# Kernel optimization log

Hardware: AMD Instinct MI355X
Metric: run time of the kernel (lower is better)

## Reference

```python
import jax, jax.numpy as jnp
import numpy as np

NUM_LAYERS = 4  # -> 9 blocks: 4 encoder + bottleneck + 4 decoder
EPS = 1e-6
SQRT2 = float(np.sqrt(2.0))
INV_SQRT3 = float(1.0 / np.sqrt(3.0))


def _block(s, v, W0, W1, Wa, Wb):
    """_SelfInteractionUNet with full_square=False, irreps = Mx0e + Mx1o.

    tensor_square of per-channel (0e+1o):
      0e: s*s ; 0e: |v|^2/sqrt(3) ; 1o: sqrt(2)*s*v ; (2e is produced by e3nn
      but irreps_out has no 2e so the Linear discards it -> omitted here).
    """
    M = s.shape[-1]
    ts0a = s * s                                    # [N, M] 0e
    ts0b = jnp.sum(v * v, axis=-1) * INV_SQRT3      # [N, M] 0e
    ts1 = SQRT2 * s[..., None] * v                  # [N, M, 3] 1o
    s_in = jnp.concatenate([s, ts0a, ts0b], axis=-1)   # [N, 3M]
    v_in = jnp.concatenate([v, ts1], axis=1)           # [N, 2M, 3]
    # irreps-segmented Linear with path (fan-in) normalization
    s2 = (s_in @ W0) * (1.0 / np.sqrt(s_in.shape[-1]))               # [N, Mo]
    v2 = jnp.einsum('ncd,co->nod', v_in, W1) * (1.0 / np.sqrt(v_in.shape[1]))  # [N, Mo, 3]
    Mo = W0.shape[-1]
    # gated MLP on invariants (0e part), silu after each layer
    h = jax.nn.silu((s2 @ Wa) * (1.0 / np.sqrt(Mo)))                 # [N, Mo]
    g = jax.nn.silu((h @ Wb) * (1.0 / np.sqrt(Mo)))                  # [N, 2Mo]
    s2 = s2 * g[:, :Mo]
    v2 = v2 * g[:, Mo:, None]
    return s2, v2


def _eq_layernorm(s, v):
    # scalars: center + RMS normalize; vectors: norm-RMS normalize (equivariant)
    s = s - jnp.mean(s, axis=-1, keepdims=True)
    s = s * jax.lax.rsqrt(jnp.mean(s * s, axis=-1, keepdims=True) + EPS)
    v = v * jax.lax.rsqrt(jnp.mean(v * v, axis=(1, 2), keepdims=True) + EPS)
    return s, v


def _unet(scalars, vectors, W0, W1, Wa, Wb):
    s, v = scalars, vectors
    skips = []
    for i in range(NUM_LAYERS):
        s, v = _block(s, v, W0[i], W1[i], Wa[i], Wb[i])
        s, v = _eq_layernorm(s, v)
        skips.append((s, v))
    s, v = _block(s, v, W0[NUM_LAYERS], W1[NUM_LAYERS], Wa[NUM_LAYERS], Wb[NUM_LAYERS])
    for j in range(NUM_LAYERS):
        ss, vs = skips[NUM_LAYERS - 1 - j]
        s, v = s + ss, v + vs
        k = NUM_LAYERS + 1 + j
        s, v = _block(s, v, W0[k], W1[k], Wa[k], Wb[k])
        if j < NUM_LAYERS - 1:  # no norm on last decoder layer (norm_last=False)
            s, v = _eq_layernorm(s, v)
    N = s.shape[0]
    return jnp.concatenate([s, v.reshape(N, -1)], axis=-1)  # [N, 4M] irreps_array layout


def setup_inputs() -> dict:
    key = jax.random.key(0)
    ks = jax.random.split(key, 6)
    N, M = 16384, 256
    return {
        'scalars': jax.random.normal(ks[0], (N, M), jnp.float32),
        'vectors': jax.random.normal(ks[1], (N, M, 3), jnp.float32),
        'W0': jax.random.normal(ks[2], (9, 3 * M, M), jnp.float32),
        'W1': jax.random.normal(ks[3], (9, 2 * M, M), jnp.float32),
        'Wa': jax.random.normal(ks[4], (9, M, M), jnp.float32),
        'Wb': jax.random.normal(ks[5], (9, M, 2 * M), jnp.float32),
    }


def reference(scalars, vectors, W0, W1, Wa, Wb):
    return _unet(scalars, vectors, W0, W1, Wa, Wb)
```

## Files before the change

kernel.cpp:

```cpp
#include <hip/hip_runtime.h>
#include <hip/hip_bf16.h>
#include <math.h>


typedef __attribute__((ext_vector_type(8))) short bf16x8;
typedef __attribute__((ext_vector_type(4))) short bf16x4;
typedef __attribute__((ext_vector_type(4))) float f32x4;
typedef __attribute__((ext_vector_type(4))) _Float16 f16x4;

__device__ __forceinline__ float bf2f(unsigned short u){
  union { unsigned int i; float f; } x; x.i = ((unsigned int)u) << 16; return x.f;
}
__device__ __forceinline__ unsigned short f2bf(float f){
  union { float f; unsigned int i; } x; x.f = f;
  unsigned int i = x.i;
  return (unsigned short)((i + 0x7fffu + ((i >> 16) & 1u)) >> 16);
}

__device__ __forceinline__ f32x4 ld4f(const float* p){ return *(const f32x4*)p; }
__device__ __forceinline__ f32x4 ld4f(const _Float16* p){
  f16x4 v = *(const f16x4*)p;
  f32x4 r;
  #pragma unroll
  for (int j = 0; j < 4; ++j) r[j] = (float)v[j];
  return r;
}

__global__ __launch_bounds__(256)
void transpose_w(const float* __restrict__ W, unsigned short* __restrict__ Wh,
                 unsigned short* __restrict__ Wl, int K, int Mo){
  __shared__ float tile[32][33];
  const int bi = blockIdx.z;
  const float* Wb = W + (size_t)bi * K * Mo;
  const size_t wo = (size_t)bi * K * Mo;
  const int k0 = blockIdx.x * 32, o0 = blockIdx.y * 32;
  const int tx = threadIdx.x & 31, ty = threadIdx.x >> 5;
  #pragma unroll
  for (int i = 0; i < 4; ++i){
    int k = ty + i * 8;
    tile[k][tx] = Wb[(size_t)(k0 + k) * Mo + o0 + tx];
  }
  __syncthreads();
  #pragma unroll
  for (int i = 0; i < 4; ++i){
    int o = ty + i * 8;
    float f = tile[tx][o];
    unsigned short h = f2bf(f);
    unsigned short l = f2bf(f - bf2f(h));
    Wh[wo + (size_t)(o0 + o) * K + k0 + tx] = h;
    Wl[wo + (size_t)(o0 + o) * K + k0 + tx] = l;
  }
}

__global__ __launch_bounds__(256)
void convert_inputs(const float* __restrict__ s, const float* __restrict__ v,
                    float* __restrict__ st, int NM){
  int i = blockIdx.x * 256 + threadIdx.x;
  if (i >= NM) return;
  st[i] = s[i];
  const float* vp = v + (size_t)i * 3;
  st[(size_t)NM + i]     = vp[0];
  st[(size_t)2 * NM + i] = vp[1];
  st[(size_t)3 * NM + i] = vp[2];
}

template<typename ST, int AMODE, int EPI>
__global__ __launch_bounds__(256)
void gemm_k(const ST* __restrict__ Ap,
            const float* __restrict__ St,
            const unsigned short* __restrict__ Bh,
            const unsigned short* __restrict__ Bl,
            int K, int Mo, int NM, float scale,
            ST* __restrict__ outf,
            const ST* __restrict__ s2g,
            const ST* __restrict__ v2g,
            float* __restrict__ stout,
            float* __restrict__ fout)
{
  __shared__ unsigned short Ah[128][40];
  __shared__ unsigned short Al[128][40];
  __shared__ unsigned short Bhs[128][40];
  __shared__ unsigned short Bls[128][40];
  const int tid  = threadIdx.x;
  const int lane = tid & 63;
  const int wave = tid >> 6;
  const int wrow = (wave >> 1) * 64;
  const int wcol = (wave & 1) * 64;
  const int row0 = blockIdx.x * 128;
  const int col0 = blockIdx.y * 128;
  int dplane = 0;
  if (AMODE == 2){ dplane = blockIdx.z; outf += (size_t)dplane * NM; }

  f32x4 acc[4][4];
  #pragma unroll
  for (int m = 0; m < 4; ++m)
    #pragma unroll
    for (int n = 0; n < 4; ++n) acc[m][n] = (f32x4){0.f, 0.f, 0.f, 0.f};

  for (int k0 = 0; k0 < K; k0 += 32){
    const int seg = k0 >> 8;
    #pragma unroll
    for (int it = 0; it < 4; ++it){
      int idx = tid + it * 256;
      int r   = idx >> 3;
      int c4  = (idx & 7) * 4;
      int gr  = row0 + r;
      int gk  = k0 + c4;
      f32x4 f;
      if (AMODE == 0){
        f = ld4f(Ap + (size_t)gr * K + gk);
      } else {
        int c = gk & 255;
        const size_t o = (size_t)gr * 256 + c;
        if (AMODE == 1){
          if (seg == 0){
            f = *(const f32x4*)(St + o);
          } else if (seg == 1){
            f32x4 x = *(const f32x4*)(St + o);
            #pragma unroll
            for (int j = 0; j < 4; ++j) f[j] = x[j] * x[j];
          } else {
            f32x4 a0 = *(const f32x4*)(St + (size_t)NM + o);
            f32x4 a1 = *(const f32x4*)(St + (size_t)2 * NM + o);
            f32x4 a2 = *(const f32x4*)(St + (size_t)3 * NM + o);
            #pragma unroll
            for (int j = 0; j < 4; ++j)
              f[j] = (a0[j]*a0[j] + a1[j]*a1[j] + a2[j]*a2[j]) * 0.57735026918962576f;
          }
        } else {
          const float* vd = St + (size_t)(1 + dplane) * NM;
          if (seg == 0){
            f = *(const f32x4*)(vd + o);
          } else {
            f32x4 sv = *(const f32x4*)(St + o);
            f32x4 vv = *(const f32x4*)(vd + o);
            #pragma unroll
            for (int j = 0; j < 4; ++j)
              f[j] = 1.41421356237309505f * sv[j] * vv[j];
          }
        }
      }
      bf16x4 hi, lo;
      #pragma unroll
      for (int j = 0; j < 4; ++j){
        unsigned short h = f2bf(f[j]);
        hi[j] = (short)h;
        lo[j] = (short)f2bf(f[j] - bf2f(h));
      }
      *(bf16x4*)(&Ah[r][c4]) = hi;
      *(bf16x4*)(&Al[r][c4]) = lo;
    }
    #pragma unroll
    for (int it = 0; it < 2; ++it){
      int idx = tid + it * 256;
      int r   = idx >> 2;
      int kc  = (idx & 3) * 8;
      const size_t o = (size_t)(col0 + r) * K + k0 + kc;
      *(bf16x8*)(&Bhs[r][kc]) = *(const bf16x8*)(Bh + o);
      *(bf16x8*)(&Bls[r][kc]) = *(const bf16x8*)(Bl + o);
    }
    __syncthreads();

    const int arow = lane & 15;
    const int kq   = (lane >> 4) * 8;
    bf16x8 ah[4], al[4], bh[4], bl[4];
    #pragma unroll
    for (int m = 0; m < 4; ++m){
      ah[m] = *(const bf16x8*)(&Ah[wrow + m*16 + arow][kq]);
      al[m] = *(const bf16x8*)(&Al[wrow + m*16 + arow][kq]);
    }
    #pragma unroll
    for (int n = 0; n < 4; ++n){
      bh[n] = *(const bf16x8*)(&Bhs[wcol + n*16 + arow][kq]);
      bl[n] = *(const bf16x8*)(&Bls[wcol + n*16 + arow][kq]);
    }
    #pragma unroll
    for (int m = 0; m < 4; ++m)
      #pragma unroll
      for (int n = 0; n < 4; ++n){
        acc[m][n] = __builtin_amdgcn_mfma_f32_16x16x32_bf16(ah[m], bh[n], acc[m][n], 0, 0, 0);
        acc[m][n] = __builtin_amdgcn_mfma_f32_16x16x32_bf16(al[m], bh[n], acc[m][n], 0, 0, 0);
        acc[m][n] = __builtin_amdgcn_mfma_f32_16x16x32_bf16(ah[m], bl[n], acc[m][n], 0, 0, 0);
      }
    __syncthreads();
  }

  #pragma unroll
  for (int m = 0; m < 4; ++m){
    #pragma unroll
    for (int n = 0; n < 4; ++n){
      const int cg = col0 + wcol + n * 16 + (lane & 15);
      #pragma unroll
      for (int j = 0; j < 4; ++j){
        const int rg = row0 + wrow + m * 16 + ((lane >> 4) * 4) + j;
        float val = acc[m][n][j] * scale;
        if (EPI == 0){
          outf[(size_t)rg * Mo + cg] = (ST)val;
        } else if (EPI == 1){
          outf[(size_t)rg * Mo + cg] = (ST)(val / (1.f + expf(-val)));
        } else {
          float gv = val / (1.f + expf(-val));
          if (cg < 256){
            float sval = (float)s2g[(size_t)rg * 256 + cg] * gv;
            if (EPI == 2) stout[(size_t)rg * 256 + cg] = sval;
            else          fout[(size_t)rg * 1024 + cg] = sval;
          } else {
            int c = cg - 256;
            #pragma unroll
            for (int d = 0; d < 3; ++d){
              float vv = (float)v2g[(size_t)d * NM + (size_t)rg * 256 + c] * gv;
              if (EPI == 2) stout[(size_t)(1 + d) * NM + (size_t)rg * 256 + c] = vv;
              else          fout[(size_t)rg * 1024 + 256 + 3 * (size_t)c + d] = vv;
            }
          }
        }
      }
    }
  }
}

__global__ __launch_bounds__(256)
void ln_k(float* __restrict__ st, _Float16* __restrict__ snap, int NM){
  const int row  = blockIdx.x * 4 + (threadIdx.x >> 6);
  const int lane = threadIdx.x & 63;
  const size_t o = (size_t)row * 256 + lane * 4;
  f32x4 sv = *(const f32x4*)(st + o);
  f32x4 v0 = *(const f32x4*)(st + (size_t)NM + o);
  f32x4 v1 = *(const f32x4*)(st + (size_t)2 * NM + o);
  f32x4 v2 = *(const f32x4*)(st + (size_t)3 * NM + o);
  float r0 = 0.f, r1 = 0.f, r2 = 0.f;
  #pragma unroll
  for (int j = 0; j < 4; ++j){
    r0 += sv[j];
    r1 += sv[j] * sv[j];
    r2 += v0[j]*v0[j] + v1[j]*v1[j] + v2[j]*v2[j];
  }
  #pragma unroll
  for (int off = 1; off < 64; off <<= 1){
    r0 += __shfl_xor(r0, off, 64);
    r1 += __shfl_xor(r1, off, 64);
    r2 += __shfl_xor(r2, off, 64);
  }
  float mu  = r0 * (1.f / 256.f);
  float var = r1 * (1.f / 256.f) - mu * mu;
  float srs = rsqrtf(var + 1e-6f);
  float vrs = rsqrtf(r2 * (1.f / 768.f) + 1e-6f);
  f32x4 so, w0, w1, w2;
  #pragma unroll
  for (int j = 0; j < 4; ++j){
    so[j] = (sv[j] - mu) * srs;
    w0[j] = v0[j] * vrs; w1[j] = v1[j] * vrs; w2[j] = v2[j] * vrs;
  }
  *(f32x4*)(st + o) = so;
  *(f32x4*)(st + (size_t)NM + o) = w0;
  *(f32x4*)(st + (size_t)2*NM + o) = w1;
  *(f32x4*)(st + (size_t)3*NM + o) = w2;
  if (snap){
    f16x4 h0, h1, h2, h3;
    #pragma unroll
    for (int j = 0; j < 4; ++j){
      h0[j] = (_Float16)so[j]; h1[j] = (_Float16)w0[j];
      h2[j] = (_Float16)w1[j]; h3[j] = (_Float16)w2[j];
    }
    *(f16x4*)(snap + o) = h0;
    *(f16x4*)(snap + (size_t)NM + o) = h1;
    *(f16x4*)(snap + (size_t)2*NM + o) = h2;
    *(f16x4*)(snap + (size_t)3*NM + o) = h3;
  }
}

__global__ __launch_bounds__(256)
void add_k(float* __restrict__ a, const _Float16* __restrict__ b, int n4){
  int i = blockIdx.x * 256 + threadIdx.x;
  if (i >= n4) return;
  f32x4 av = ((const f32x4*)a)[i];
  f16x4 bv = ((const f16x4*)b)[i];
  #pragma unroll
  for (int j = 0; j < 4; ++j) av[j] += (float)bv[j];
  ((f32x4*)a)[i] = av;
}

template<typename ST>
static void run_unet(const unsigned short* W0h, const unsigned short* W0l,
                     const unsigned short* W1h, const unsigned short* W1l,
                     const unsigned short* Wah, const unsigned short* Wal,
                     const unsigned short* Wbh, const unsigned short* Wbl,
                     float* state, ST* s2, ST* v2, ST* h, _Float16* skips,
                     float* out, int N, int NM, hipStream_t stream){
  dim3 blk(256);
  const float c_s2 = 1.f / sqrtf(768.f);
  const float c_v2 = 1.f / sqrtf(512.f);
  const float c_hg = 1.f / 16.f;
  const int gx = N / 128;

  auto run_block = [&](int i, bool fin){
    const unsigned short* w0h = W0h + (size_t)i * 768 * 256;
    const unsigned short* w0l = W0l + (size_t)i * 768 * 256;
    const unsigned short* w1h = W1h + (size_t)i * 512 * 256;
    const unsigned short* w1l = W1l + (size_t)i * 512 * 256;
    const unsigned short* wah = Wah + (size_t)i * 256 * 256;
    const unsigned short* wal = Wal + (size_t)i * 256 * 256;
    const unsigned short* wbh = Wbh + (size_t)i * 256 * 512;
    const unsigned short* wbl = Wbl + (size_t)i * 256 * 512;
    gemm_k<ST,1,0><<<dim3(gx, 2, 1), blk, 0, stream>>>(nullptr, state, w0h, w0l, 768, 256, NM, c_s2,
                                                       s2, nullptr, nullptr, nullptr, nullptr);
    gemm_k<ST,2,0><<<dim3(gx, 2, 3), blk, 0, stream>>>(nullptr, state, w1h, w1l, 512, 256, NM, c_v2,
                                                       v2, nullptr, nullptr, nullptr, nullptr);
    gemm_k<ST,0,1><<<dim3(gx, 2, 1), blk, 0, stream>>>(s2, nullptr, wah, wal, 256, 256, NM, c_hg,
                                                       h, nullptr, nullptr, nullptr, nullptr);
    if (!fin)
      gemm_k<ST,0,2><<<dim3(gx, 4, 1), blk, 0, stream>>>(h, nullptr, wbh, wbl, 256, 512, NM, c_hg,
                                                         nullptr, s2, v2, state, nullptr);
    else
      gemm_k<ST,0,3><<<dim3(gx, 4, 1), blk, 0, stream>>>(h, nullptr, wbh, wbl, 256, 512, NM, c_hg,
                                                         nullptr, s2, v2, nullptr, out);
  };

  for (int i = 0; i < 4; ++i){
    run_block(i, false);
    ln_k<<<dim3(N/4), blk, 0, stream>>>(state, skips + (size_t)i * 4 * NM, NM);
  }
  run_block(4, false);
  for (int j = 0; j < 4; ++j){
    add_k<<<dim3(NM / 256), blk, 0, stream>>>(state, skips + (size_t)(3 - j) * 4 * NM, NM);
    run_block(5 + j, j == 3);
    if (j < 3) ln_k<<<dim3(N/4), blk, 0, stream>>>(state, nullptr, NM);
  }
}

extern "C" void kernel_launch(void* const* d_in, const int* in_sizes, int n_in,
                              void* d_out, int out_size, void* d_ws, size_t ws_size,
                              hipStream_t stream){
  const float* s_in = (const float*)d_in[0];
  const float* v_in = (const float*)d_in[1];
  const float* W0 = (const float*)d_in[2];
  const float* W1 = (const float*)d_in[3];
  const float* Wa = (const float*)d_in[4];
  const float* Wb = (const float*)d_in[5];
  const int Mdim = 256;
  const int N  = in_sizes[0] / Mdim;
  const int NM = N * Mdim;

  char* ws = (char*)d_ws;
  size_t off = 0;
  auto allocS = [&](size_t elems){ unsigned short* p = (unsigned short*)(ws + off); off += elems * 2; return p; };
  unsigned short* W0h = allocS((size_t)9 * 768 * 256);
  unsigned short* W0l = allocS((size_t)9 * 768 * 256);
  unsigned short* W1h = allocS((size_t)9 * 512 * 256);
  unsigned short* W1l = allocS((size_t)9 * 512 * 256);
  unsigned short* Wah = allocS((size_t)9 * 256 * 256);
  unsigned short* Wal = allocS((size_t)9 * 256 * 256);
  unsigned short* Wbh = allocS((size_t)9 * 256 * 512);
  unsigned short* Wbl = allocS((size_t)9 * 256 * 512);
  const size_t weights_bytes = off;
  const size_t skips_bytes   = (size_t)16 * NM * 2;
  const size_t temps32_bytes = (size_t)5 * NM * 4;
  const bool use_f32 = (ws_size == 0) ||
                       (ws_size >= weights_bytes + temps32_bytes + skips_bytes);

  float* state = (float*)d_out;

  dim3 blk(256);
  transpose_w<<<dim3(768/32, 256/32, 9), blk, 0, stream>>>(W0, W0h, W0l, 768, 256);
  transpose_w<<<dim3(512/32, 256/32, 9), blk, 0, stream>>>(W1, W1h, W1l, 512, 256);
  transpose_w<<<dim3(256/32, 256/32, 9), blk, 0, stream>>>(Wa, Wah, Wal, 256, 256);
  transpose_w<<<dim3(256/32, 512/32, 9), blk, 0, stream>>>(Wb, Wbh, Wbl, 256, 512);
  convert_inputs<<<dim3(NM/256), blk, 0, stream>>>(s_in, v_in, state, NM);

  if (use_f32){
    float* s2 = (float*)(ws + off);
    float* v2 = s2 + NM;
    float* h  = v2 + (size_t)3 * NM;
    _Float16* skips = (_Float16*)(h + NM);
    run_unet<float>(W0h, W0l, W1h, W1l, Wah, Wal, Wbh, Wbl,
                    state, s2, v2, h, skips, (float*)d_out, N, NM, stream);
  } else {
    _Float16* s2 = (_Float16*)(ws + off);
    _Float16* v2 = s2 + NM;
    _Float16* h  = v2 + (size_t)3 * NM;
    _Float16* skips = h + NM;
    run_unet<_Float16>(W0h, W0l, W1h, W1l, Wah, Wal, Wbh, Wbl,
                       state, s2, v2, h, skips, (float*)d_out, N, NM, stream);
  }
}
```

Measured before the change: 1.964 ms.

## Shrink GEMM tiles to 64x64 with K-step 64 and fuse skip-add into loads

```diff
diff --git a/kernel.cpp b/kernel.cpp
--- a/kernel.cpp
+++ b/kernel.cpp
@@ -65,9 +65,10 @@
 }
 
 template<typename ST, int AMODE, int EPI>
-__global__ __launch_bounds__(256)
+__global__ __launch_bounds__(256, 4)
 void gemm_k(const ST* __restrict__ Ap,
             const float* __restrict__ St,
+            const _Float16* __restrict__ skip,
             const unsigned short* __restrict__ Bh,
             const unsigned short* __restrict__ Bl,
             int K, int Mo, int NM, float scale,
@@ -77,75 +78,91 @@
             float* __restrict__ stout,
             float* __restrict__ fout)
 {
-  __shared__ unsigned short Ah[128][40];
-  __shared__ unsigned short Al[128][40];
-  __shared__ unsigned short Bhs[128][40];
-  __shared__ unsigned short Bls[128][40];
+  __shared__ unsigned short Ah[64][72];
+  __shared__ unsigned short Al[64][72];
+  __shared__ unsigned short Bhs[64][72];
+  __shared__ unsigned short Bls[64][72];
   const int tid  = threadIdx.x;
   const int lane = tid & 63;
   const int wave = tid >> 6;
-  const int wrow = (wave >> 1) * 64;
-  const int wcol = (wave & 1) * 64;
-  const int row0 = blockIdx.x * 128;
-  const int col0 = blockIdx.y * 128;
+  const int wm = (wave >> 1) * 32;
+  const int wn = (wave & 1) * 32;
+  const int row0 = blockIdx.x * 64;
+  const int col0 = blockIdx.y * 64;
   int dplane = 0;
   if (AMODE == 2){ dplane = blockIdx.z; outf += (size_t)dplane * NM; }
-
-  f32x4 acc[4][4];
-  #pragma unroll
-  for (int m = 0; m < 4; ++m)
-    #pragma unroll
-    for (int n = 0; n < 4; ++n) acc[m][n] = (f32x4){0.f, 0.f, 0.f, 0.f};
-
-  for (int k0 = 0; k0 < K; k0 += 32){
+  const bool sk = (skip != nullptr);
+
+  f32x4 acc[2][2];
+  #pragma unroll
+  for (int m = 0; m < 2; ++m)
+    #pragma unroll
+    for (int n = 0; n < 2; ++n) acc[m][n] = (f32x4){0.f, 0.f, 0.f, 0.f};
+
+  for (int k0 = 0; k0 < K; k0 += 64){
     const int seg = k0 >> 8;
     #pragma unroll
     for (int it = 0; it < 4; ++it){
       int idx = tid + it * 256;
-      int r   = idx >> 3;
-      int c4  = (idx & 7) * 4;
+      int r   = idx >> 4;
+      int c4  = (idx & 15) * 4;
       int gr  = row0 + r;
       int gk  = k0 + c4;
       f32x4 f;
       if (AMODE == 0){
         f = ld4f(Ap + (size_t)gr * K + gk);
       } else {
-        int c = gk & 255;
+        const int c = gk & 255;
         const size_t o = (size_t)gr * 256 + c;
         if (AMODE == 1){
-          if (seg == 0){
-            f = *(const f32x4*)(St + o);
-          } else if (seg == 1){
+          if (seg <= 1){
             f32x4 x = *(const f32x4*)(St + o);
-            #pragma unroll
-            for (int j = 0; j < 4; ++j) f[j] = x[j] * x[j];
+            if (sk){ f32x4 y = ld4f(skip + o);
+              #pragma unroll
+              for (int j = 0; j < 4; ++j) x[j] += y[j]; }
+            if (seg == 0) f = x;
+            else {
+              #pragma unroll
+              for (int j = 0; j < 4; ++j) f[j] = x[j] * x[j];
+            }
           } else {
             f32x4 a0 = *(const f32x4*)(St + (size_t)NM + o);
             f32x4 a1 = *(const f32x4*)(St + (size_t)2 * NM + o);
             f32x4 a2 = *(const f32x4*)(St + (size_t)3 * NM + o);
+            if (sk){
+              f32x4 b0 = ld4f(skip + (size_t)NM + o);
+              f32x4 b1 = ld4f(skip + (size_t)2 * NM + o);
+              f32x4 b2 = ld4f(skip + (size_t)3 * NM + o);
+              #pragma unroll
+              for (int j = 0; j < 4; ++j){ a0[j]+=b0[j]; a1[j]+=b1[j]; a2[j]+=b2[j]; }
+            }
             #pragma unroll
             for (int j = 0; j < 4; ++j)
               f[j] = (a0[j]*a0[j] + a1[j]*a1[j] + a2[j]*a2[j]) * 0.57735026918962576f;
           }
         } else {
-          const float* vd = St + (size_t)(1 + dplane) * NM;
-          if (seg == 0){
-            f = *(const f32x4*)(vd + o);
-          } else {
-            f32x4 sv = *(const f32x4*)(St + o);
-            f32x4 vv = *(const f32x4*)(vd + o);
+          f32x4 x = *(const f32x4*)(St + (size_t)(1 + dplane) * NM + o);
+          if (sk){ f32x4 y = ld4f(skip + (size_t)(1 + dplane) * NM + o);
+            #pragma unroll
+            for (int j = 0; j < 4; ++j) x[j] += y[j]; }
+          if (seg == 0) f = x;
+          else {
+            f32x4 s = *(const f32x4*)(St + o);
+            if (sk){ f32x4 y = ld4f(skip + o);
+              #pragma unroll
+              for (int j = 0; j < 4; ++j) s[j] += y[j]; }
             #pragma unroll
             for (int j = 0; j < 4; ++j)
-              f[j] = 1.41421356237309505f * sv[j] * vv[j];
+              f[j] = 1.41421356237309505f * s[j] * x[j];
           }
         }
       }
       bf16x4 hi, lo;
       #pragma unroll
       for (int j = 0; j < 4; ++j){
-        unsigned short h = f2bf(f[j]);
-        hi[j] = (short)h;
-        lo[j] = (short)f2bf(f[j] - bf2f(h));
+        unsigned short hbits = f2bf(f[j]);
+        hi[j] = (short)hbits;
+        lo[j] = (short)f2bf(f[j] - bf2f(hbits));
       }
       *(bf16x4*)(&Ah[r][c4]) = hi;
       *(bf16x4*)(&Al[r][c4]) = lo;
@@ -153,8 +170,8 @@
     #pragma unroll
     for (int it = 0; it < 2; ++it){
       int idx = tid + it * 256;
-      int r   = idx >> 2;
-      int kc  = (idx & 3) * 8;
+      int r   = idx >> 3;
+      int kc  = (idx & 7) * 8;
       const size_t o = (size_t)(col0 + r) * K + k0 + kc;
       *(bf16x8*)(&Bhs[r][kc]) = *(const bf16x8*)(Bh + o);
       *(bf16x8*)(&Bls[r][kc]) = *(const bf16x8*)(Bl + o);
@@ -163,36 +180,40 @@
 
     const int arow = lane & 15;
     const int kq   = (lane >> 4) * 8;
-    bf16x8 ah[4], al[4], bh[4], bl[4];
-    #pragma unroll
-    for (int m = 0; m < 4; ++m){
-      ah[m] = *(const bf16x8*)(&Ah[wrow + m*16 + arow][kq]);
-      al[m] = *(const bf16x8*)(&Al[wrow + m*16 + arow][kq]);
-    }
-    #pragma unroll
-    for (int n = 0; n < 4; ++n){
-      bh[n] = *(const bf16x8*)(&Bhs[wcol + n*16 + arow][kq]);
-      bl[n] = *(const bf16x8*)(&Bls[wcol + n*16 + arow][kq]);
-    }
-    #pragma unroll
-    for (int m = 0; m < 4; ++m)
-      #pragma unroll
-      for (int n = 0; n < 4; ++n){
-        acc[m][n] = __builtin_amdgcn_mfma_f32_16x16x32_bf16(ah[m], bh[n], acc[m][n], 0, 0, 0);
-        acc[m][n] = __builtin_amdgcn_mfma_f32_16x16x32_bf16(al[m], bh[n], acc[m][n], 0, 0, 0);
-        acc[m][n] = __builtin_amdgcn_mfma_f32_16x16x32_bf16(ah[m], bl[n], acc[m][n], 0, 0, 0);
-      }
+    #pragma unroll
+    for (int ks = 0; ks < 2; ++ks){
+      const int kb = ks * 32 + kq;
+      bf16x8 ah[2], al[2], bh[2], bl[2];
+      #pragma unroll
+      for (int m = 0; m < 2; ++m){
+        ah[m] = *(const bf16x8*)(&Ah[wm + m*16 + arow][kb]);
+        al[m] = *(const bf16x8*)(&Al[wm + m*16 + arow][kb]);
+      }
+      #pragma unroll
+      for (int n = 0; n < 2; ++n){
+        bh[n] = *(const bf16x8*)(&Bhs[wn + n*16 + arow][kb]);
+        bl[n] = *(const bf16x8*)(&Bls[wn + n*16 + arow][kb]);
+      }
+      #pragma unroll
+      for (int m = 0; m < 2; ++m)
+        #pragma unroll
+        for (int n = 0; n < 2; ++n){
+          acc[m][n] = __builtin_amdgcn_mfma_f32_16x16x32_bf16(ah[m], bh[n], acc[m][n], 0, 0, 0);
+          acc[m][n] = __builtin_amdgcn_mfma_f32_16x16x32_bf16(al[m], bh[n], acc[m][n], 0, 0, 0);
+          acc[m][n] = __builtin_amdgcn_mfma_f32_16x16x32_bf16(ah[m], bl[n], acc[m][n], 0, 0, 0);
+        }
+    }
     __syncthreads();
   }
 
   #pragma unroll
-  for (int m = 0; m < 4; ++m){
-    #pragma unroll
-    for (int n = 0; n < 4; ++n){
-      const int cg = col0 + wcol + n * 16 + (lane & 15);
+  for (int m = 0; m < 2; ++m){
+    #pragma unroll
+    for (int n = 0; n < 2; ++n){
+      const int cg = col0 + wn + n * 16 + (lane & 15);
       #pragma unroll
       for (int j = 0; j < 4; ++j){
-        const int rg = row0 + wrow + m * 16 + ((lane >> 4) * 4) + j;
+        const int rg = row0 + wm + m * 16 + ((lane >> 4) * 4) + j;
         float val = acc[m][n][j] * scale;
         if (EPI == 0){
           outf[(size_t)rg * Mo + cg] = (ST)val;
@@ -269,17 +290,6 @@
   }
 }
 
-__global__ __launch_bounds__(256)
-void add_k(float* __restrict__ a, const _Float16* __restrict__ b, int n4){
-  int i = blockIdx.x * 256 + threadIdx.x;
-  if (i >= n4) return;
-  f32x4 av = ((const f32x4*)a)[i];
-  f16x4 bv = ((const f16x4*)b)[i];
-  #pragma unroll
-  for (int j = 0; j < 4; ++j) av[j] += (float)bv[j];
-  ((f32x4*)a)[i] = av;
-}
-
 template<typename ST>
 static void run_unet(const unsigned short* W0h, const unsigned short* W0l,
                      const unsigned short* W1h, const unsigned short* W1l,
@@ -291,9 +301,9 @@
   const float c_s2 = 1.f / sqrtf(768.f);
   const float c_v2 = 1.f / sqrtf(512.f);
   const float c_hg = 1.f / 16.f;
-  const int gx = N / 128;
-
-  auto run_block = [&](int i, bool fin){
+  const int gx = N / 64;
+
+  auto run_block = [&](int i, bool fin, const _Float16* skip){
     const unsigned short* w0h = W0h + (size_t)i * 768 * 256;
     const unsigned short* w0l = W0l + (size_t)i * 768 * 256;
     const unsigned short* w1h = W1h + (size_t)i * 512 * 256;
@@ -302,28 +312,27 @@
     const unsigned short* wal = Wal + (size_t)i * 256 * 256;
     const unsigned short* wbh = Wbh + (size_t)i * 256 * 512;
     const unsigned short* wbl = Wbl + (size_t)i * 256 * 512;
-    gemm_k<ST,1,0><<<dim3(gx, 2, 1), blk, 0, stream>>>(nullptr, state, w0h, w0l, 768, 256, NM, c_s2,
+    gemm_k<ST,1,0><<<dim3(gx, 4, 1), blk, 0, stream>>>(nullptr, state, skip, w0h, w0l, 768, 256, NM, c_s2,
                                                        s2, nullptr, nullptr, nullptr, nullptr);
-    gemm_k<ST,2,0><<<dim3(gx, 2, 3), blk, 0, stream>>>(nullptr, state, w1h, w1l, 512, 256, NM, c_v2,
+    gemm_k<ST,2,0><<<dim3(gx, 4, 3), blk, 0, stream>>>(nullptr, state, skip, w1h, w1l, 512, 256, NM, c_v2,
                                                        v2, nullptr, nullptr, nullptr, nullptr);
-    gemm_k<ST,0,1><<<dim3(gx, 2, 1), blk, 0, stream>>>(s2, nullptr, wah, wal, 256, 256, NM, c_hg,
+    gemm_k<ST,0,1><<<dim3(gx, 4, 1), blk, 0, stream>>>(s2, nullptr, nullptr, wah, wal, 256, 256, NM, c_hg,
                                                        h, nullptr, nullptr, nullptr, nullptr);
     if (!fin)
-      gemm_k<ST,0,2><<<dim3(gx, 4, 1), blk, 0, stream>>>(h, nullptr, wbh, wbl, 256, 512, NM, c_hg,
+      gemm_k<ST,0,2><<<dim3(gx, 8, 1), blk, 0, stream>>>(h, nullptr, nullptr, wbh, wbl, 256, 512, NM, c_hg,
                                                          nullptr, s2, v2, state, nullptr);
     else
-      gemm_k<ST,0,3><<<dim3(gx, 4, 1), blk, 0, stream>>>(h, nullptr, wbh, wbl, 256, 512, NM, c_hg,
+      gemm_k<ST,0,3><<<dim3(gx, 8, 1), blk, 0, stream>>>(h, nullptr, nullptr, wbh, wbl, 256, 512, NM, c_hg,
                                                          nullptr, s2, v2, nullptr, out);
   };
 
   for (int i = 0; i < 4; ++i){
-    run_block(i, false);
+    run_block(i, false, nullptr);
     ln_k<<<dim3(N/4), blk, 0, stream>>>(state, skips + (size_t)i * 4 * NM, NM);
   }
-  run_block(4, false);
+  run_block(4, false, nullptr);
   for (int j = 0; j < 4; ++j){
-    add_k<<<dim3(NM / 256), blk, 0, stream>>>(state, skips + (size_t)(3 - j) * 4 * NM, NM);
-    run_block(5 + j, j == 3);
+    run_block(5 + j, j == 3, skips + (size_t)(3 - j) * 4 * NM);
     if (j < 3) ln_k<<<dim3(N/4), blk, 0, stream>>>(state, nullptr, NM);
   }
 }
```

Result: no change. 1.993 ms (+1.5%).
